# Kernel tuning notes

Measured on AMD Instinct MI355X. Metric: run time of the kernel, lower is better.

## Reference

```python
import jax, jax.numpy as jnp
import numpy as np

N_NODES = 100000
N_EDGES = 1600000
IN_SIZE = 512
HID_SIZE = 256
OUT_SIZE = 40
K_STEPS = 10
ALPHA = 0.1


def setup_inputs() -> dict:
    key = jax.random.key(0)
    ks = jax.random.split(key, 8)
    features = jax.random.normal(ks[0], (N_NODES, IN_SIZE), dtype=jnp.float32)
    src = jax.random.randint(ks[1], (N_EDGES,), 0, N_NODES, dtype=jnp.int64)
    dst = jax.random.randint(ks[2], (N_EDGES,), 0, N_NODES, dtype=jnp.int64)
    # MLP params (Kaiming-ish scale)
    W1 = jax.random.normal(ks[3], (IN_SIZE, HID_SIZE), dtype=jnp.float32) / np.sqrt(IN_SIZE)
    b1 = jnp.zeros((HID_SIZE,), dtype=jnp.float32)
    W2 = jax.random.normal(ks[4], (HID_SIZE, OUT_SIZE), dtype=jnp.float32) / np.sqrt(HID_SIZE)
    b2 = jnp.zeros((OUT_SIZE,), dtype=jnp.float32)
    return {"features": features, "src": src, "dst": dst,
            "W1": W1, "b1": b1, "W2": W2, "b2": b2}


def reference(features, src, dst, W1, b1, W2, b2):
    # --- MLP encoder (dropout is identity in eval mode) ---
    h = jax.nn.relu(features @ W1 + b1)
    h = h @ W2 + b2  # [N, out_size]

    # --- Symmetric normalization (DGL APPNPConv, edge_weight=None) ---
    ones_e = jnp.ones((src.shape[0],), dtype=h.dtype)
    deg_out = jax.ops.segment_sum(ones_e, src, num_segments=N_NODES)
    deg_in = jax.ops.segment_sum(ones_e, dst, num_segments=N_NODES)
    norm_src = jnp.power(jnp.clip(deg_out, 1.0), -0.5)[:, None]  # D_out^{-1/2}
    norm_dst = jnp.power(jnp.clip(deg_in, 1.0), -0.5)[:, None]   # D_in^{-1/2}

    # --- k=10 APPNP propagation: h <- (1-a) * D^{-1/2} A D^{-1/2} h + a * h0 ---
    h0 = h

    def step(h, _):
        msg = (h * norm_src)[src]                                  # gather [E, out]
        agg = jax.ops.segment_sum(msg, dst, num_segments=N_NODES)  # scatter-add
        h = (1.0 - ALPHA) * (agg * norm_dst) + ALPHA * h0
        return h, None

    h, _ = jax.lax.scan(step, h, None, length=K_STEPS)
    return h
```

## Files before the change

kernel.cpp:

```cpp
#include <hip/hip_runtime.h>

#define N_NODES 100000
#define N_EDGES 1600000
#define IN_SIZE 512
#define HID_SIZE 256
#define OUT_SIZE 40
#define K_STEPS 10
#define ALPHA 0.1f

#define NCH 250
#define CH_E 6400
#define NBUK 391
#define NRS 8
#define HRS 12544
#define NCS 16
#define CS_E 100000

typedef _Float16 half8 __attribute__((ext_vector_type(8)));
typedef float f32x4 __attribute__((ext_vector_type(4)));

struct __align__(8) Entry { int s; int d; };

__global__ __launch_bounds__(512) void hist_pass(const int* __restrict__ dst,
                                                 int* __restrict__ cnt) {
    __shared__ int h[NBUK];
    const int t = threadIdx.x, c = blockIdx.x;
    for (int j = t; j < NBUK; j += 512) h[j] = 0;
    __syncthreads();
    const int4* d4 = (const int4*)(dst + c * CH_E);
    for (int i = t; i < CH_E / 4; i += 512) {
        const int4 v = d4[i];
        atomicAdd(&h[v.x >> 8], 1);
        atomicAdd(&h[v.y >> 8], 1);
        atomicAdd(&h[v.z >> 8], 1);
        atomicAdd(&h[v.w >> 8], 1);
    }
    __syncthreads();
    for (int j = t; j < NBUK; j += 512) cnt[c * NBUK + j] = h[j];
}

__global__ __launch_bounds__(512) void bucket_scan(const int* __restrict__ cnt,
                                                   int* __restrict__ off,
                                                   int* __restrict__ boff) {
    __shared__ int tot[512];
    const int b = threadIdx.x;
    int s = 0;
    if (b < NBUK)
        for (int c = 0; c < NCH; ++c) s += cnt[c * NBUK + b];
    tot[b] = s;
    __syncthreads();
    for (int o = 1; o < 512; o <<= 1) {
        const int v = (b >= o) ? tot[b - o] : 0;
        __syncthreads();
        tot[b] += v;
        __syncthreads();
    }
    if (b < NBUK) {
        int run = tot[b] - s;
        boff[b] = run;
        for (int c = 0; c < NCH; ++c) { off[c * NBUK + b] = run; run += cnt[c * NBUK + b]; }
        if (b == NBUK - 1) boff[NBUK] = tot[b];
    }
}

__global__ __launch_bounds__(512) void scatter_pass(const int* __restrict__ src,
                                                    const int* __restrict__ dst,
                                                    const int* __restrict__ off,
                                                    Entry* __restrict__ ebuf) {
    __shared__ int cur[NBUK];
    const int t = threadIdx.x, c = blockIdx.x;
    for (int j = t; j < NBUK; j += 512) cur[j] = off[c * NBUK + j];
    __syncthreads();
    const int4* s4 = (const int4*)(src + c * CH_E);
    const int4* d4 = (const int4*)(dst + c * CH_E);
    for (int i = t; i < CH_E / 4; i += 512) {
        const int4 sv = s4[i];
        const int4 dv = d4[i];
        Entry e;
        int p;
        p = atomicAdd(&cur[dv.x >> 8], 1); e.s = sv.x; e.d = dv.x; ebuf[p] = e;
        p = atomicAdd(&cur[dv.y >> 8], 1); e.s = sv.y; e.d = dv.y; ebuf[p] = e;
        p = atomicAdd(&cur[dv.z >> 8], 1); e.s = sv.z; e.d = dv.z; ebuf[p] = e;
        p = atomicAdd(&cur[dv.w >> 8], 1); e.s = sv.w; e.d = dv.w; ebuf[p] = e;
    }
}

__global__ __launch_bounds__(256) void bucket_csr(const Entry* __restrict__ ebuf,
                                                  const int* __restrict__ boff,
                                                  int* __restrict__ rowp,
                                                  float* __restrict__ ndst,
                                                  int* __restrict__ csr) {
    __shared__ int hist[256];
    __shared__ int pref[256];
    __shared__ int cur[256];
    const int t = threadIdx.x, b = blockIdx.x;
    const int beg = boff[b], end = boff[b + 1];
    hist[t] = 0;
    __syncthreads();
    for (int i = beg + t; i < end; i += 256)
        atomicAdd(&hist[ebuf[i].d & 255], 1);
    __syncthreads();
    const int h = hist[t];
    pref[t] = h;
    __syncthreads();
    for (int o = 1; o < 256; o <<= 1) {
        const int v = (t >= o) ? pref[t - o] : 0;
        __syncthreads();
        pref[t] += v;
        __syncthreads();
    }
    const int val = beg + pref[t] - h;
    const int n = (b << 8) + t;
    if (n <= N_NODES) rowp[n] = val;
    if (n < N_NODES) ndst[n] = 1.0f / sqrtf((float)max(h, 1));
    cur[t] = val;
    __syncthreads();
    for (int i = beg + t; i < end; i += 256) {
        const Entry e = ebuf[i];
        const int pos = atomicAdd(&cur[e.d & 255], 1);
        csr[pos] = e.s;
    }
}

__global__ __launch_bounds__(512) void degsrc_part(const int* __restrict__ src,
                                                   int* __restrict__ partial) {
    __shared__ int h[HRS];
    const int t = threadIdx.x;
    const int r = blockIdx.x & (NRS - 1);
    const int c = blockIdx.x >> 3;
    const int base = r * HRS;
    for (int j = t; j < HRS; j += 512) h[j] = 0;
    __syncthreads();
    const int4* s4 = (const int4*)(src + (size_t)c * CS_E);
    for (int i = t; i < CS_E / 4; i += 512) {
        const int4 v = s4[i];
        unsigned u;
        u = (unsigned)(v.x - base); if (u < HRS) atomicAdd(&h[u], 1);
        u = (unsigned)(v.y - base); if (u < HRS) atomicAdd(&h[u], 1);
        u = (unsigned)(v.z - base); if (u < HRS) atomicAdd(&h[u], 1);
        u = (unsigned)(v.w - base); if (u < HRS) atomicAdd(&h[u], 1);
    }
    __syncthreads();
    for (int j = t; j < HRS; j += 512) partial[(size_t)c * (NRS * HRS) + base + j] = h[j];
}

__global__ __launch_bounds__(256) void nsrc_reduce(const int* __restrict__ partial,
                                                   float* __restrict__ nsrc) {
    const int n = blockIdx.x * 256 + threadIdx.x;
    int s = 0;
#pragma unroll
    for (int c = 0; c < NCS; ++c) s += partial[(size_t)c * (NRS * HRS) + n];
    if (n < N_NODES) nsrc[n] = 1.0f / sqrtf((float)max(s, 1));
}

__global__ __launch_bounds__(256) void prep_w1t(const float* __restrict__ W1,
                                                unsigned short* __restrict__ w1t) {
    int idx = blockIdx.x * 256 + threadIdx.x;
    if (idx < IN_SIZE * HID_SIZE) {
        int n = idx >> 9;
        int k = idx & 511;
        _Float16 h = (_Float16)W1[(size_t)k * HID_SIZE + n];
        w1t[idx] = *(unsigned short*)&h;
    }
}

__global__ __launch_bounds__(512) void gemm1_f16(const float* __restrict__ X,
                                                 const unsigned short* __restrict__ w1t,
                                                 const float* __restrict__ b1,
                                                 _Float16* __restrict__ h1) {
    __shared__ __align__(16) _Float16 sA[128 * 64];
    __shared__ __align__(16) _Float16 sB[256 * 64];

    const int t    = threadIdx.x;
    const int lane = t & 63;
    const int w    = t >> 6;
    const int wr   = w >> 2;
    const int wc   = w & 3;
    const int n0   = blockIdx.x * 128;

    f32x4 acc[4][4];
#pragma unroll
    for (int i = 0; i < 4; ++i)
#pragma unroll
        for (int j = 0; j < 4; ++j) acc[i][j] = (f32x4)0.f;

    const int lo = lane & 15;
    const int hi = lane >> 4;
    const int l7 = lane & 7;

    for (int kk = 0; kk < IN_SIZE; kk += 64) {
        __syncthreads();
#pragma unroll
        for (int i = 0; i < 2; ++i) {
            int id  = t + i * 512;
            int row = id >> 3;
            int ch  = id & 7;
            int gr  = n0 + row;
            float4 x0 = make_float4(0.f, 0.f, 0.f, 0.f), x1 = x0;
            if (gr < N_NODES) {
                const float* p = X + (size_t)gr * IN_SIZE + kk + ch * 8;
                x0 = ((const float4*)p)[0];
                x1 = ((const float4*)p)[1];
            }
            half8 hv;
            hv[0] = (_Float16)x0.x; hv[1] = (_Float16)x0.y;
            hv[2] = (_Float16)x0.z; hv[3] = (_Float16)x0.w;
            hv[4] = (_Float16)x1.x; hv[5] = (_Float16)x1.y;
            hv[6] = (_Float16)x1.z; hv[7] = (_Float16)x1.w;
            *(half8*)&sA[row * 64 + ((ch ^ (row & 7)) << 3)] = hv;
        }
#pragma unroll
        for (int i = 0; i < 4; ++i) {
            int id = t + i * 512;
            int n  = id >> 3;
            int ch = id & 7;
            uint4 v = *(const uint4*)(w1t + (size_t)n * IN_SIZE + kk + ch * 8);
            *(uint4*)&sB[n * 64 + ((ch ^ (n & 7)) << 3)] = v;
        }
        __syncthreads();
#pragma unroll
        for (int s = 0; s < 2; ++s) {
            const int chs = ((s * 4 + hi) ^ l7) << 3;
            half8 af[4], bf[4];
#pragma unroll
            for (int f = 0; f < 4; ++f)
                af[f] = *(const half8*)&sA[(wr * 64 + f * 16 + lo) * 64 + chs];
#pragma unroll
            for (int f = 0; f < 4; ++f)
                bf[f] = *(const half8*)&sB[(wc * 64 + f * 16 + lo) * 64 + chs];
#pragma unroll
            for (int fi = 0; fi < 4; ++fi)
#pragma unroll
                for (int fj = 0; fj < 4; ++fj)
                    acc[fi][fj] = __builtin_amdgcn_mfma_f32_16x16x32_f16(
                        af[fi], bf[fj], acc[fi][fj], 0, 0, 0);
        }
    }

    float b1v[4];
#pragma unroll
    for (int fj = 0; fj < 4; ++fj) b1v[fj] = b1[wc * 64 + fj * 16 + lo];
#pragma unroll
    for (int fi = 0; fi < 4; ++fi) {
#pragma unroll
        for (int fj = 0; fj < 4; ++fj) {
            const int col = wc * 64 + fj * 16 + lo;
#pragma unroll
            for (int r = 0; r < 4; ++r) {
                int grow = n0 + wr * 64 + fi * 16 + hi * 4 + r;
                if (grow < N_NODES) {
                    float v = acc[fi][fj][r] + b1v[fj];
                    v = fmaxf(v, 0.f);
                    h1[(size_t)grow * HID_SIZE + col] = (_Float16)v;
                }
            }
        }
    }
}

__global__ __launch_bounds__(256) void gemm2(const _Float16* __restrict__ h1,
                                             const float* __restrict__ W2,
                                             const float* __restrict__ b2,
                                             float* __restrict__ h0) {
    __shared__ __align__(16) float sW2t[40 * 260];
    __shared__ __align__(16) unsigned short sH[64 * 264];

    const int t  = threadIdx.x;
    const int n0 = blockIdx.x * 64;

    for (int idx = t; idx < HID_SIZE * OUT_SIZE; idx += 256) {
        int c = idx / OUT_SIZE;
        int o = idx - c * OUT_SIZE;
        sW2t[o * 260 + c] = W2[idx];
    }
#pragma unroll
    for (int i = 0; i < 8; ++i) {
        int id  = t + i * 256;
        int row = id >> 5;
        int ch  = id & 31;
        uint4 v = make_uint4(0, 0, 0, 0);
        if (n0 + row < N_NODES)
            v = *(const uint4*)(h1 + (size_t)(n0 + row) * HID_SIZE + ch * 8);
        *(uint4*)&sH[row * 264 + ch * 8] = v;
    }
    __syncthreads();

    const int r2 = t >> 2;
    const int q  = t & 3;
    const int o0 = q * 10;
    float acc2[10];
#pragma unroll
    for (int m = 0; m < 10; ++m) acc2[m] = b2[o0 + m];

    for (int c = 0; c < HID_SIZE; c += 8) {
        uint4 hv = *(const uint4*)&sH[r2 * 264 + c];
        const _Float16* hp = (const _Float16*)&hv;
        float f[8];
#pragma unroll
        for (int j = 0; j < 8; ++j) f[j] = (float)hp[j];
#pragma unroll
        for (int m = 0; m < 10; ++m) {
            const float4 w0 = *(const float4*)&sW2t[(o0 + m) * 260 + c];
            const float4 w1 = *(const float4*)&sW2t[(o0 + m) * 260 + c + 4];
            acc2[m] += f[0] * w0.x + f[1] * w0.y + f[2] * w0.z + f[3] * w0.w
                     + f[4] * w1.x + f[5] * w1.y + f[6] * w1.z + f[7] * w1.w;
        }
    }
    if (n0 + r2 < N_NODES) {
        float* dstp = h0 + (size_t)(n0 + r2) * OUT_SIZE + o0;
#pragma unroll
        for (int m = 0; m < 10; ++m) dstp[m] = acc2[m];
    }
}

__global__ __launch_bounds__(320) void g0_init(const float* __restrict__ h0,
                                               const float* __restrict__ nsrc,
                                               _Float16* __restrict__ g) {
    const int tid = threadIdx.x;
    const int ln  = tid / 5;
    const int q   = tid - ln * 5;
    const int n   = blockIdx.x * 64 + ln;
    if (n >= N_NODES) return;
    const float ns = nsrc[n];
    const f32x4 a = *(const f32x4*)(h0 + (size_t)n * OUT_SIZE + q * 8);
    const f32x4 b = *(const f32x4*)(h0 + (size_t)n * OUT_SIZE + q * 8 + 4);
    half8 gv;
    gv[0] = (_Float16)(ns * a[0]); gv[1] = (_Float16)(ns * a[1]);
    gv[2] = (_Float16)(ns * a[2]); gv[3] = (_Float16)(ns * a[3]);
    gv[4] = (_Float16)(ns * b[0]); gv[5] = (_Float16)(ns * b[1]);
    gv[6] = (_Float16)(ns * b[2]); gv[7] = (_Float16)(ns * b[3]);
    *(half8*)(g + (size_t)n * 64 + q * 8) = gv;
}

__global__ __launch_bounds__(320) void appnp_step6(const _Float16* __restrict__ gin,
                                                   const float* __restrict__ h0,
                                                   const int* __restrict__ rowp,
                                                   const int* __restrict__ csr,
                                                   const float* __restrict__ nsrc,
                                                   const float* __restrict__ ndst,
                                                   _Float16* __restrict__ gout,
                                                   float* __restrict__ hout,
                                                   int last) {
    const int tid = threadIdx.x;
    const int ln  = tid / 5;
    const int q   = tid - ln * 5;
    const int n   = blockIdx.x * 64 + ln;
    if (n >= N_NODES) return;

    const int beg = rowp[n];
    const int end = rowp[n + 1];
    const _Float16* gq = gin + q * 8;

    float acc[8];
#pragma unroll
    for (int j = 0; j < 8; ++j) acc[j] = 0.f;

    int e = beg;
    {
        int alim = (beg + 3) & ~3;
        if (alim > end) alim = end;
        for (; e < alim; ++e) {
            const int s0 = csr[e];
            const half8 v0 = *(const half8*)(gq + (size_t)s0 * 64);
#pragma unroll
            for (int j = 0; j < 8; ++j) acc[j] += (float)v0[j];
        }
    }
    for (; e + 4 <= end; e += 4) {
        const int4 s4 = *(const int4*)(csr + e);
        const half8 v0 = *(const half8*)(gq + (size_t)s4.x * 64);
        const half8 v1 = *(const half8*)(gq + (size_t)s4.y * 64);
        const half8 v2 = *(const half8*)(gq + (size_t)s4.z * 64);
        const half8 v3 = *(const half8*)(gq + (size_t)s4.w * 64);
#pragma unroll
        for (int j = 0; j < 8; ++j)
            acc[j] += (float)v0[j] + (float)v1[j] + (float)v2[j] + (float)v3[j];
    }
    for (; e < end; ++e) {
        const int s0 = csr[e];
        const half8 v0 = *(const half8*)(gq + (size_t)s0 * 64);
#pragma unroll
        for (int j = 0; j < 8; ++j) acc[j] += (float)v0[j];
    }

    const float nd = (1.0f - ALPHA) * ndst[n];
    const f32x4 h0a = *(const f32x4*)(h0 + (size_t)n * OUT_SIZE + q * 8);
    const f32x4 h0b = *(const f32x4*)(h0 + (size_t)n * OUT_SIZE + q * 8 + 4);
    float r[8];
    r[0] = nd * acc[0] + ALPHA * h0a[0]; r[1] = nd * acc[1] + ALPHA * h0a[1];
    r[2] = nd * acc[2] + ALPHA * h0a[2]; r[3] = nd * acc[3] + ALPHA * h0a[3];
    r[4] = nd * acc[4] + ALPHA * h0b[0]; r[5] = nd * acc[5] + ALPHA * h0b[1];
    r[6] = nd * acc[6] + ALPHA * h0b[2]; r[7] = nd * acc[7] + ALPHA * h0b[3];

    if (last) {
        f32x4 ra, rb;
        ra[0] = r[0]; ra[1] = r[1]; ra[2] = r[2]; ra[3] = r[3];
        rb[0] = r[4]; rb[1] = r[5]; rb[2] = r[6]; rb[3] = r[7];
        *(f32x4*)(hout + (size_t)n * OUT_SIZE + q * 8) = ra;
        *(f32x4*)(hout + (size_t)n * OUT_SIZE + q * 8 + 4) = rb;
    } else {
        const float ns = nsrc[n];
        half8 gv;
#pragma unroll
        for (int j = 0; j < 8; ++j) gv[j] = (_Float16)(ns * r[j]);
        *(half8*)(gout + (size_t)n * 64 + q * 8) = gv;
    }
}

extern "C" void kernel_launch(void* const* d_in, const int* in_sizes, int n_in,
                              void* d_out, int out_size, void* d_ws, size_t ws_size,
                              hipStream_t stream) {
    const float* X   = (const float*)d_in[0];
    const int*   src = (const int*)d_in[1];
    const int*   dst = (const int*)d_in[2];
    const float* W1  = (const float*)d_in[3];
    const float* b1  = (const float*)d_in[4];
    const float* W2  = (const float*)d_in[5];
    const float* b2  = (const float*)d_in[6];
    float* out = (float*)d_out;

    char* ws = (char*)d_ws;
    size_t off = 0;
    auto alloc = [&](size_t bytes) -> void* {
        void* p = ws + off;
        off = (off + bytes + 255) & ~(size_t)255;
        return p;
    };
    float*    h0  = (float*)alloc((size_t)N_NODES * OUT_SIZE * 4);
    _Float16* h1  = (_Float16*)alloc((size_t)N_NODES * HID_SIZE * 2);
    _Float16* gA  = (_Float16*)alloc((size_t)N_NODES * 64 * 2);
    _Float16* gB  = (_Float16*)alloc((size_t)N_NODES * 64 * 2);
    Entry* ebuf    = (Entry*)alloc((size_t)N_EDGES * 8);
    int*   partial = (int*)alloc((size_t)NCS * NRS * HRS * 4);
    float* nsrc = (float*)alloc((size_t)N_NODES * 4);
    float* ndst = (float*)alloc((size_t)N_NODES * 4);
    int* rowp   = (int*)alloc((size_t)(N_NODES + 2) * 4);
    int* csr    = (int*)alloc((size_t)N_EDGES * 4);
    int* cnt    = (int*)alloc((size_t)NCH * NBUK * 4);
    int* offb   = (int*)alloc((size_t)NCH * NBUK * 4);
    int* boff   = (int*)alloc((size_t)(NBUK + 1) * 4);
    unsigned short* w1t = (unsigned short*)alloc((size_t)IN_SIZE * HID_SIZE * 2);

    const int pgrid = (N_NODES + 63) / 64;

    hist_pass<<<NCH, 512, 0, stream>>>(dst, cnt);
    bucket_scan<<<1, 512, 0, stream>>>(cnt, offb, boff);
    scatter_pass<<<NCH, 512, 0, stream>>>(src, dst, offb, ebuf);
    bucket_csr<<<NBUK, 256, 0, stream>>>(ebuf, boff, rowp, ndst, csr);
    degsrc_part<<<NRS * NCS, 512, 0, stream>>>(src, partial);
    nsrc_reduce<<<(NRS * HRS) / 256, 256, 0, stream>>>(partial, nsrc);

    prep_w1t<<<(IN_SIZE * HID_SIZE + 255) / 256, 256, 0, stream>>>(W1, w1t);
    gemm1_f16<<<(N_NODES + 127) / 128, 512, 0, stream>>>(X, w1t, b1, h1);
    gemm2<<<(N_NODES + 63) / 64, 256, 0, stream>>>(h1, W2, b2, h0);

    g0_init<<<pgrid, 320, 0, stream>>>(h0, nsrc, gA);

    const _Float16* gin = gA;
    for (int s = 0; s < K_STEPS; ++s) {
        const int last = (s == K_STEPS - 1) ? 1 : 0;
        _Float16* gout = (s & 1) ? gA : gB;
        appnp_step6<<<pgrid, 320, 0, stream>>>(gin, h0, rowp, csr, nsrc, ndst,
                                               gout, out, last);
        gin = gout;
    }
}
```

Baseline: 568.5 us.

## Slice propagation features into 8 node-major planes for cache-local gathers

Reorganizes the propagated feature buffer from one 64-half row per node into 8 separate slices of 5 useful halves (padded to 8) per node. Each block processes one slice, with the slice index taken from the low bits of the block id, so that the gathered working set per slice (1.6 MB) can stay resident in cache during the random neighbor gathers. It also stores alpha*h0 in the same sliced fp16 layout instead of reading fp32 h0. In exchange, every edge index and rowp entry is now read 8 times per step instead of once, and each 16-byte gather carries 3 padding halves. The last step writes 5 floats per thread with scalar stores, and the fp16 alpha*h0 adds some rounding error.

```diff
diff --git a/kernel.cpp b/kernel.cpp
--- a/kernel.cpp
+++ b/kernel.cpp
@@ -313,97 +313,101 @@
     }
 }
 
-__global__ __launch_bounds__(320) void g0_init(const float* __restrict__ h0,
-                                               const float* __restrict__ nsrc,
-                                               _Float16* __restrict__ g) {
-    const int tid = threadIdx.x;
-    const int ln  = tid / 5;
-    const int q   = tid - ln * 5;
-    const int n   = blockIdx.x * 64 + ln;
+__global__ __launch_bounds__(256) void g0_init_sliced(const float* __restrict__ h0,
+                                                      const float* __restrict__ nsrc,
+                                                      _Float16* __restrict__ g,
+                                                      _Float16* __restrict__ h0aS) {
+    const int n = blockIdx.x * 256 + threadIdx.x;
     if (n >= N_NODES) return;
     const float ns = nsrc[n];
-    const f32x4 a = *(const f32x4*)(h0 + (size_t)n * OUT_SIZE + q * 8);
-    const f32x4 b = *(const f32x4*)(h0 + (size_t)n * OUT_SIZE + q * 8 + 4);
-    half8 gv;
-    gv[0] = (_Float16)(ns * a[0]); gv[1] = (_Float16)(ns * a[1]);
-    gv[2] = (_Float16)(ns * a[2]); gv[3] = (_Float16)(ns * a[3]);
-    gv[4] = (_Float16)(ns * b[0]); gv[5] = (_Float16)(ns * b[1]);
-    gv[6] = (_Float16)(ns * b[2]); gv[7] = (_Float16)(ns * b[3]);
-    *(half8*)(g + (size_t)n * 64 + q * 8) = gv;
-}
-
-__global__ __launch_bounds__(320) void appnp_step6(const _Float16* __restrict__ gin,
-                                                   const float* __restrict__ h0,
-                                                   const int* __restrict__ rowp,
-                                                   const int* __restrict__ csr,
-                                                   const float* __restrict__ nsrc,
-                                                   const float* __restrict__ ndst,
-                                                   _Float16* __restrict__ gout,
-                                                   float* __restrict__ hout,
-                                                   int last) {
-    const int tid = threadIdx.x;
-    const int ln  = tid / 5;
-    const int q   = tid - ln * 5;
-    const int n   = blockIdx.x * 64 + ln;
+    float v[40];
+#pragma unroll
+    for (int i = 0; i < 10; ++i) {
+        const f32x4 x = *(const f32x4*)(h0 + (size_t)n * OUT_SIZE + i * 4);
+        v[i * 4 + 0] = x[0]; v[i * 4 + 1] = x[1];
+        v[i * 4 + 2] = x[2]; v[i * 4 + 3] = x[3];
+    }
+#pragma unroll
+    for (int s = 0; s < 8; ++s) {
+        half8 gv, av;
+#pragma unroll
+        for (int k = 0; k < 5; ++k) {
+            const float f = v[s * 5 + k];
+            gv[k] = (_Float16)(ns * f);
+            av[k] = (_Float16)(ALPHA * f);
+        }
+        gv[5] = (_Float16)0.f; gv[6] = (_Float16)0.f; gv[7] = (_Float16)0.f;
+        av[5] = (_Float16)0.f; av[6] = (_Float16)0.f; av[7] = (_Float16)0.f;
+        *(half8*)(g    + ((size_t)s * N_NODES + n) * 8) = gv;
+        *(half8*)(h0aS + ((size_t)s * N_NODES + n) * 8) = av;
+    }
+}
+
+__global__ __launch_bounds__(256) void appnp_sliced(const _Float16* __restrict__ gin,
+                                                    const _Float16* __restrict__ h0aS,
+                                                    const int* __restrict__ rowp,
+                                                    const int* __restrict__ csr,
+                                                    const float* __restrict__ nsrc,
+                                                    const float* __restrict__ ndst,
+                                                    _Float16* __restrict__ gout,
+                                                    float* __restrict__ hout,
+                                                    int last) {
+    const int s = blockIdx.x & 7;
+    const int n = (blockIdx.x >> 3) * 256 + threadIdx.x;
     if (n >= N_NODES) return;
+    const _Float16* gs = gin + (size_t)s * N_NODES * 8;
 
     const int beg = rowp[n];
     const int end = rowp[n + 1];
-    const _Float16* gq = gin + q * 8;
-
-    float acc[8];
-#pragma unroll
-    for (int j = 0; j < 8; ++j) acc[j] = 0.f;
-
+
+    float a0 = 0.f, a1 = 0.f, a2 = 0.f, a3 = 0.f, a4 = 0.f;
     int e = beg;
     {
         int alim = (beg + 3) & ~3;
         if (alim > end) alim = end;
         for (; e < alim; ++e) {
-            const int s0 = csr[e];
-            const half8 v0 = *(const half8*)(gq + (size_t)s0 * 64);
-#pragma unroll
-            for (int j = 0; j < 8; ++j) acc[j] += (float)v0[j];
+            const half8 v = *(const half8*)(gs + (size_t)csr[e] * 8);
+            a0 += (float)v[0]; a1 += (float)v[1]; a2 += (float)v[2];
+            a3 += (float)v[3]; a4 += (float)v[4];
         }
     }
     for (; e + 4 <= end; e += 4) {
         const int4 s4 = *(const int4*)(csr + e);
-        const half8 v0 = *(const half8*)(gq + (size_t)s4.x * 64);
-        const half8 v1 = *(const half8*)(gq + (size_t)s4.y * 64);
-        const half8 v2 = *(const half8*)(gq + (size_t)s4.z * 64);
-        const half8 v3 = *(const half8*)(gq + (size_t)s4.w * 64);
-#pragma unroll
-        for (int j = 0; j < 8; ++j)
-            acc[j] += (float)v0[j] + (float)v1[j] + (float)v2[j] + (float)v3[j];
+        const half8 v0 = *(const half8*)(gs + (size_t)s4.x * 8);
+        const half8 v1 = *(const half8*)(gs + (size_t)s4.y * 8);
+        const half8 v2 = *(const half8*)(gs + (size_t)s4.z * 8);
+        const half8 v3 = *(const half8*)(gs + (size_t)s4.w * 8);
+        a0 += (float)v0[0] + (float)v1[0] + (float)v2[0] + (float)v3[0];
+        a1 += (float)v0[1] + (float)v1[1] + (float)v2[1] + (float)v3[1];
+        a2 += (float)v0[2] + (float)v1[2] + (float)v2[2] + (float)v3[2];
+        a3 += (float)v0[3] + (float)v1[3] + (float)v2[3] + (float)v3[3];
+        a4 += (float)v0[4] + (float)v1[4] + (float)v2[4] + (float)v3[4];
     }
     for (; e < end; ++e) {
-        const int s0 = csr[e];
-        const half8 v0 = *(const half8*)(gq + (size_t)s0 * 64);
-#pragma unroll
-        for (int j = 0; j < 8; ++j) acc[j] += (float)v0[j];
+        const half8 v = *(const half8*)(gs + (size_t)csr[e] * 8);
+        a0 += (float)v[0]; a1 += (float)v[1]; a2 += (float)v[2];
+        a3 += (float)v[3]; a4 += (float)v[4];
     }
 
     const float nd = (1.0f - ALPHA) * ndst[n];
-    const f32x4 h0a = *(const f32x4*)(h0 + (size_t)n * OUT_SIZE + q * 8);
-    const f32x4 h0b = *(const f32x4*)(h0 + (size_t)n * OUT_SIZE + q * 8 + 4);
-    float r[8];
-    r[0] = nd * acc[0] + ALPHA * h0a[0]; r[1] = nd * acc[1] + ALPHA * h0a[1];
-    r[2] = nd * acc[2] + ALPHA * h0a[2]; r[3] = nd * acc[3] + ALPHA * h0a[3];
-    r[4] = nd * acc[4] + ALPHA * h0b[0]; r[5] = nd * acc[5] + ALPHA * h0b[1];
-    r[6] = nd * acc[6] + ALPHA * h0b[2]; r[7] = nd * acc[7] + ALPHA * h0b[3];
+    const half8 ha = *(const half8*)(h0aS + ((size_t)s * N_NODES + n) * 8);
+    const float r0 = nd * a0 + (float)ha[0];
+    const float r1 = nd * a1 + (float)ha[1];
+    const float r2 = nd * a2 + (float)ha[2];
+    const float r3 = nd * a3 + (float)ha[3];
+    const float r4 = nd * a4 + (float)ha[4];
 
     if (last) {
-        f32x4 ra, rb;
-        ra[0] = r[0]; ra[1] = r[1]; ra[2] = r[2]; ra[3] = r[3];
-        rb[0] = r[4]; rb[1] = r[5]; rb[2] = r[6]; rb[3] = r[7];
-        *(f32x4*)(hout + (size_t)n * OUT_SIZE + q * 8) = ra;
-        *(f32x4*)(hout + (size_t)n * OUT_SIZE + q * 8 + 4) = rb;
+        float* o = hout + (size_t)n * OUT_SIZE + s * 5;
+        o[0] = r0; o[1] = r1; o[2] = r2; o[3] = r3; o[4] = r4;
     } else {
         const float ns = nsrc[n];
         half8 gv;
-#pragma unroll
-        for (int j = 0; j < 8; ++j) gv[j] = (_Float16)(ns * r[j]);
-        *(half8*)(gout + (size_t)n * 64 + q * 8) = gv;
+        gv[0] = (_Float16)(ns * r0); gv[1] = (_Float16)(ns * r1);
+        gv[2] = (_Float16)(ns * r2); gv[3] = (_Float16)(ns * r3);
+        gv[4] = (_Float16)(ns * r4);
+        gv[5] = (_Float16)0.f; gv[6] = (_Float16)0.f; gv[7] = (_Float16)0.f;
+        *(half8*)(gout + ((size_t)s * N_NODES + n) * 8) = gv;
     }
 }
 
@@ -426,10 +430,11 @@
         off = (off + bytes + 255) & ~(size_t)255;
         return p;
     };
-    float*    h0  = (float*)alloc((size_t)N_NODES * OUT_SIZE * 4);
-    _Float16* h1  = (_Float16*)alloc((size_t)N_NODES * HID_SIZE * 2);
-    _Float16* gA  = (_Float16*)alloc((size_t)N_NODES * 64 * 2);
-    _Float16* gB  = (_Float16*)alloc((size_t)N_NODES * 64 * 2);
+    float*    h0   = (float*)alloc((size_t)N_NODES * OUT_SIZE * 4);
+    _Float16* h1   = (_Float16*)alloc((size_t)N_NODES * HID_SIZE * 2);
+    _Float16* gSA  = (_Float16*)alloc((size_t)8 * N_NODES * 8 * 2);
+    _Float16* gSB  = (_Float16*)alloc((size_t)8 * N_NODES * 8 * 2);
+    _Float16* h0aS = (_Float16*)alloc((size_t)8 * N_NODES * 8 * 2);
     Entry* ebuf    = (Entry*)alloc((size_t)N_EDGES * 8);
     int*   partial = (int*)alloc((size_t)NCS * NRS * HRS * 4);
     float* nsrc = (float*)alloc((size_t)N_NODES * 4);
@@ -441,8 +446,6 @@
     int* boff   = (int*)alloc((size_t)(NBUK + 1) * 4);
     unsigned short* w1t = (unsigned short*)alloc((size_t)IN_SIZE * HID_SIZE * 2);
 
-    const int pgrid = (N_NODES + 63) / 64;
-
     hist_pass<<<NCH, 512, 0, stream>>>(dst, cnt);
     bucket_scan<<<1, 512, 0, stream>>>(cnt, offb, boff);
     scatter_pass<<<NCH, 512, 0, stream>>>(src, dst, offb, ebuf);
@@ -454,14 +457,16 @@
     gemm1_f16<<<(N_NODES + 127) / 128, 512, 0, stream>>>(X, w1t, b1, h1);
     gemm2<<<(N_NODES + 63) / 64, 256, 0, stream>>>(h1, W2, b2, h0);
 
-    g0_init<<<pgrid, 320, 0, stream>>>(h0, nsrc, gA);
-
-    const _Float16* gin = gA;
+    const int ngrid256 = (N_NODES + 255) / 256;
+    g0_init_sliced<<<ngrid256, 256, 0, stream>>>(h0, nsrc, gSA, h0aS);
+
+    const int sgrid = ngrid256 * 8;
+    const _Float16* gin = gSA;
     for (int s = 0; s < K_STEPS; ++s) {
         const int last = (s == K_STEPS - 1) ? 1 : 0;
-        _Float16* gout = (s & 1) ? gA : gB;
-        appnp_step6<<<pgrid, 320, 0, stream>>>(gin, h0, rowp, csr, nsrc, ndst,
-                                               gout, out, last);
+        _Float16* gout = (s & 1) ? gSA : gSB;
+        appnp_sliced<<<sgrid, 256, 0, stream>>>(gin, h0aS, rowp, csr, nsrc, ndst,
+                                                gout, out, last);
         gin = gout;
     }
 }
```

Result: slower. 1.029 ms (+81.0%).
